# Performance work log

Measured on AMD Instinct MI355X. Metric: run time of the kernel, lower is better.

The kernel has to match this reference:

```python
import jax, jax.numpy as jnp
import numpy as np

N_NODES = 50000
N_EDGES = 800000
D_IN = 256
D_OUT = 128
EPS = 1e-9


def setup_inputs() -> dict:
    key = jax.random.key(0)
    ks = jax.random.split(key, 6)
    feat = jax.random.normal(ks[0], (N_NODES, D_IN), dtype=jnp.float32)
    edge_row = jax.random.randint(ks[1], (N_EDGES,), 0, N_NODES)
    edge_col = jax.random.randint(ks[2], (N_EDGES,), 0, N_NODES)
    # normalized adjacency values (positive, ~1/degree scale)
    edge_val = jax.random.uniform(ks[3], (N_EDGES,), dtype=jnp.float32) / 16.0
    # xavier_uniform for Linear(dim_in, dim_out) weights, stored as [D_IN, D_OUT]
    limit = float(np.sqrt(6.0 / (D_IN + D_OUT)))
    W0 = jax.random.uniform(ks[4], (D_IN, D_OUT), minval=-limit, maxval=limit, dtype=jnp.float32)
    W1 = jax.random.uniform(ks[5], (D_IN, D_OUT), minval=-limit, maxval=limit, dtype=jnp.float32)
    zeros = jnp.zeros((D_OUT,), dtype=jnp.float32)
    ones = jnp.ones((D_OUT,), dtype=jnp.float32)
    return {
        "feat": feat,
        "W0": W0, "b0": zeros, "scale0": ones, "offset0": zeros,
        "W1": W1, "b1": zeros, "scale1": ones, "offset1": zeros,
        "edge_row": edge_row, "edge_col": edge_col, "edge_val": edge_val,
    }


def _spmm(edge_row, edge_col, edge_val, x):
    # out[r] += val * x[c] for each edge (r, c, val)  -- sparse adj @ x
    msgs = edge_val[:, None] * x[edge_col]  # [E, D]
    return jax.ops.segment_sum(msgs, edge_row, num_segments=N_NODES)


def _feat_trans(x, W, b, scale, offset):
    h = jax.nn.relu(x @ W + b)  # [N, D_OUT]
    mean = jnp.mean(h, axis=1, keepdims=True)
    var = jnp.var(h, axis=1, keepdims=True) + EPS  # unbiased=False (population var)
    return (h - mean) * scale * jax.lax.rsqrt(var) + offset


def reference(feat, W0, b0, scale0, offset0, W1, b1, scale1, offset1,
              edge_row, edge_col, edge_val):
    # non-first-layer path: feat_hop = [X, A @ X] (order=1), dropout p=0 is identity
    hop1 = _spmm(edge_row, edge_col, edge_val, feat)
    f0 = _feat_trans(feat, W0, b0, scale0, offset0)
    f1 = _feat_trans(hop1, W1, b1, scale1, offset1)
    return jnp.concatenate([f0, f1], axis=1)  # aggr == 'concat'
```

## Files before the change

### kernel.cpp

```cpp
#include <hip/hip_runtime.h>

#define N_NODES 50000
#define N_EDGES 800000
#define D_IN    256
#define D_OUT   128
#define EPS     1e-9f
#define CAP     64
#define PAD     88

#define SCATTER_BLOCKS 196
#define GEMM_MBLKS     391

typedef __attribute__((ext_vector_type(8))) short bf16x8;
typedef __attribute__((ext_vector_type(4))) float floatx4;

__device__ __forceinline__ ushort f2bf(float x) {
    unsigned u = __float_as_uint(x);
    u += 0x7fffu + ((u >> 16) & 1u);
    return (ushort)(u >> 16);
}

#define CNT_BLOCKS 49
#define WB_BLOCKS  32
__global__ __launch_bounds__(256) void prep_small(
    const float* __restrict__ W0, const float* __restrict__ W1,
    ushort* __restrict__ Wb, int* __restrict__ cnt)
{
    int bid = blockIdx.x;
    int t   = threadIdx.x;
    if (bid < CNT_BLOCKS) {
        int idx4 = bid * 256 + t;
        if (idx4 < 12500)
            *(int4*)&cnt[idx4 * 4] = make_int4(0, 0, 0, 0);
    } else {
        int g  = (bid - CNT_BLOCKS) * 256 + t;
        int n  = g >> 5;
        int kq = g & 31;
        const float* W = (n < 128) ? W0 : W1;
        int nn = n & 127;
        union { ushort us[8]; uint4 v; } tmp;
#pragma unroll
        for (int j = 0; j < 8; ++j)
            tmp.us[j] = f2bf(W[(size_t)(kq * 8 + j) * D_OUT + nn]);
        *(uint4*)&Wb[(size_t)n * D_IN + kq * 8] = tmp.v;
    }
}

__global__ __launch_bounds__(256, 3) void gemm_scatter(
    const float* __restrict__ feat, const ushort* __restrict__ Wb,
    const float* __restrict__ bias, const float* __restrict__ scale,
    const float* __restrict__ offset,
    float* __restrict__ out, ushort* __restrict__ Y1,
    const int* __restrict__ er, const int* __restrict__ ec,
    const float* __restrict__ ev, int* __restrict__ cnt,
    int2* __restrict__ slot2)
{
    __shared__ ushort As[128 * PAD];
    __shared__ ushort Bs[128 * PAD];

    const int t = threadIdx.x;

    if (blockIdx.x < SCATTER_BLOCKS) {
        int ebase = blockIdx.x * 4096;
        int   rr[16], cc[16];
        float vv[16];
#pragma unroll
        for (int u = 0; u < 16; ++u) {
            int e = ebase + u * 256 + t;
            bool ok = (e < N_EDGES);
            rr[u] = ok ? er[e] : -1;
            cc[u] = ok ? ec[e] : 0;
            vv[u] = ok ? ev[e] : 0.f;
        }
#pragma unroll
        for (int u = 0; u < 16; ++u) {
            if (rr[u] >= 0) {
                int pos = atomicAdd(&cnt[rr[u]], 1);
                if (pos < CAP)
                    slot2[(size_t)rr[u] * CAP + pos] =
                        make_int2(cc[u], __float_as_int(vv[u]));
            }
        }
        return;
    }

    const int gbid = blockIdx.x - SCATTER_BLOCKS;
    const int half = gbid / GEMM_MBLKS;
    const int mblk = gbid % GEMM_MBLKS;
    const int wave = t >> 6, lane = t & 63;
    const int quad = lane >> 4, l16 = lane & 15;
    const int m0   = mblk * 128;
    const int n0   = half * 128;

    floatx4 acc[2][8];
#pragma unroll
    for (int mt = 0; mt < 2; ++mt)
#pragma unroll
        for (int nt = 0; nt < 8; ++nt)
            acc[mt][nt] = (floatx4){0.f, 0.f, 0.f, 0.f};

    for (int kt = 0; kt < D_IN; kt += 64) {
#pragma unroll
        for (int i = 0; i < 4; ++i) {
            int g = t + i * 256;
            int row = g >> 3, kq = g & 7;
            int grow = m0 + row;
            union { ushort us[8]; uint4 v; } tmp;
            tmp.v = make_uint4(0u, 0u, 0u, 0u);
            if (grow < N_NODES) {
                const float* p = &feat[(size_t)grow * D_IN + kt + kq * 8];
                float4 v0 = *(const float4*)p;
                float4 v1 = *(const float4*)(p + 4);
                tmp.us[0] = f2bf(v0.x); tmp.us[1] = f2bf(v0.y);
                tmp.us[2] = f2bf(v0.z); tmp.us[3] = f2bf(v0.w);
                tmp.us[4] = f2bf(v1.x); tmp.us[5] = f2bf(v1.y);
                tmp.us[6] = f2bf(v1.z); tmp.us[7] = f2bf(v1.w);
            }
            *(uint4*)&As[row * PAD + kq * 8] = tmp.v;
        }
#pragma unroll
        for (int i = 0; i < 4; ++i) {
            int g = t + i * 256;
            int row = g >> 3, kq = g & 7;
            *(uint4*)&Bs[row * PAD + kq * 8] =
                *(const uint4*)&Wb[(size_t)(n0 + row) * D_IN + kt + kq * 8];
        }
        __syncthreads();

#pragma unroll
        for (int kk = 0; kk < 64; kk += 32) {
            bf16x8 a[2], b[8];
#pragma unroll
            for (int mt = 0; mt < 2; ++mt)
                a[mt] = *(bf16x8*)&As[(wave * 32 + mt * 16 + l16) * PAD + kk + quad * 8];
#pragma unroll
            for (int nt = 0; nt < 8; ++nt)
                b[nt] = *(bf16x8*)&Bs[(nt * 16 + l16) * PAD + kk + quad * 8];
#pragma unroll
            for (int mt = 0; mt < 2; ++mt)
#pragma unroll
                for (int nt = 0; nt < 8; ++nt)
                    acc[mt][nt] = __builtin_amdgcn_mfma_f32_16x16x32_bf16(
                        a[mt], b[nt], acc[mt][nt], 0, 0, 0);
        }
        __syncthreads();
    }

    if (half == 0) {
        float bb[8], sc[8], of[8];
#pragma unroll
        for (int nt = 0; nt < 8; ++nt) {
            bb[nt] = bias[nt * 16 + l16];
            sc[nt] = scale[nt * 16 + l16];
            of[nt] = offset[nt * 16 + l16];
        }
#pragma unroll
        for (int mt = 0; mt < 2; ++mt)
#pragma unroll
            for (int i = 0; i < 4; ++i) {
                float h[8], s = 0.f, q = 0.f;
#pragma unroll
                for (int nt = 0; nt < 8; ++nt) {
                    h[nt] = fmaxf(acc[mt][nt][i] + bb[nt], 0.f);
                    s += h[nt];
                    q += h[nt] * h[nt];
                }
#pragma unroll
                for (int m = 1; m < 16; m <<= 1) {
                    s += __shfl_xor(s, m);
                    q += __shfl_xor(q, m);
                }
                float mean = s * (1.f / 128.f);
                float inv  = rsqrtf(q * (1.f / 128.f) - mean * mean + EPS);
                int row = m0 + wave * 32 + mt * 16 + quad * 4 + i;
                if (row < N_NODES) {
#pragma unroll
                    for (int nt = 0; nt < 8; ++nt)
                        out[(size_t)row * 256 + nt * 16 + l16] =
                            (h[nt] - mean) * sc[nt] * inv + of[nt];
                }
            }
    } else {
#pragma unroll
        for (int mt = 0; mt < 2; ++mt)
#pragma unroll
            for (int i = 0; i < 4; ++i) {
                int row = m0 + wave * 32 + mt * 16 + quad * 4 + i;
                if (row < N_NODES) {
#pragma unroll
                    for (int nt = 0; nt < 8; ++nt)
                        Y1[(size_t)row * D_OUT + nt * 16 + l16] =
                            f2bf(acc[mt][nt][i]);
                }
            }
    }
}

__global__ __launch_bounds__(256) void spmm_gather_ln(
    const int* __restrict__ cnt, const int2* __restrict__ slot2,
    const ushort* __restrict__ Y,
    const float* __restrict__ bias, const float* __restrict__ scale,
    const float* __restrict__ offset, float* __restrict__ out)
{
    int row  = blockIdx.x * 4 + (threadIdx.x >> 6);
    int lane = threadIdx.x & 63;
    if (row >= N_NODES) return;

    int n = cnt[row];
    n = n < CAP ? n : CAP;

    int   c = 0;
    float v = 0.f;
    if (lane < n) {
        int2 p = slot2[(size_t)row * CAP + lane];
        c = p.x;
        v = __int_as_float(p.y);
    }

    float ax = 0.f, ay = 0.f;
    int j = 0;
    for (; j + 8 <= n; j += 8) {
        unsigned yv[8]; float vv[8];
#pragma unroll
        for (int u = 0; u < 8; ++u) {
            int cj = __shfl(c, j + u);
            vv[u]  = __shfl(v, j + u);
            yv[u]  = *(const unsigned*)&Y[(size_t)cj * D_OUT + lane * 2];
        }
#pragma unroll
        for (int u = 0; u < 8; ++u) {
            ax = fmaf(vv[u], __uint_as_float(yv[u] << 16), ax);
            ay = fmaf(vv[u], __uint_as_float(yv[u] & 0xffff0000u), ay);
        }
    }
    for (; j < n; ++j) {
        int   cj = __shfl(c, j);
        float vj = __shfl(v, j);
        unsigned yv = *(const unsigned*)&Y[(size_t)cj * D_OUT + lane * 2];
        ax = fmaf(vj, __uint_as_float(yv << 16), ax);
        ay = fmaf(vj, __uint_as_float(yv & 0xffff0000u), ay);
    }

    int cidx = lane * 2;
    float h0 = fmaxf(ax + bias[cidx + 0], 0.f);
    float h1 = fmaxf(ay + bias[cidx + 1], 0.f);
    float s = h0 + h1, q = h0 * h0 + h1 * h1;
#pragma unroll
    for (int m = 1; m < 64; m <<= 1) {
        s += __shfl_xor(s, m);
        q += __shfl_xor(q, m);
    }
    float mean = s * (1.f / 128.f);
    float var  = q * (1.f / 128.f) - mean * mean + EPS;
    float inv  = rsqrtf(var);
    float2 o;
    o.x = (h0 - mean) * scale[cidx + 0] * inv + offset[cidx + 0];
    o.y = (h1 - mean) * scale[cidx + 1] * inv + offset[cidx + 1];
    *(float2*)&out[(size_t)row * 256 + 128 + cidx] = o;
}

extern "C" void kernel_launch(void* const* d_in, const int* in_sizes, int n_in,
                              void* d_out, int out_size, void* d_ws, size_t ws_size,
                              hipStream_t stream)
{
    const float* feat = (const float*)d_in[0];
    const float* W0   = (const float*)d_in[1];
    const float* b0   = (const float*)d_in[2];
    const float* s0   = (const float*)d_in[3];
    const float* o0   = (const float*)d_in[4];
    const float* W1   = (const float*)d_in[5];
    const float* b1   = (const float*)d_in[6];
    const float* s1   = (const float*)d_in[7];
    const float* o1   = (const float*)d_in[8];
    const int*   er   = (const int*)d_in[9];
    const int*   ec   = (const int*)d_in[10];
    const float* ev   = (const float*)d_in[11];
    float* out = (float*)d_out;

    char*   wsb   = (char*)d_ws;
    ushort* Wb    = (ushort*)(wsb);
    ushort* Y1    = (ushort*)(wsb + 131072);
    int*    cnt   = (int*)   (wsb + 12931072);
    int2*   slot2 = (int2*)  (wsb + 13131072);

    prep_small<<<CNT_BLOCKS + WB_BLOCKS, 256, 0, stream>>>(W0, W1, Wb, cnt);

    gemm_scatter<<<SCATTER_BLOCKS + 2 * GEMM_MBLKS, 256, 0, stream>>>(
        feat, Wb, b0, s0, o0, out, Y1, er, ec, ev, cnt, slot2);

    spmm_gather_ln<<<(N_NODES + 3) / 4, 256, 0, stream>>>(
        cnt, slot2, Y1, b1, s1, o1, out);
}
```

Before: 204.0 us.

## Bucket edges by 128-row groups with shared-memory histogram and local CSR build

Replaces the per-row global atomic slot scatter with a two-level scheme. Each scatter block builds a shared-memory histogram over 128-row buckets, reserves space with one global atomic per bucket, and writes packed (local row, column, value) entries. The gather kernel then loads one bucket into LDS, builds a CSR layout with a prefix scan, and processes its rows. This is meant to cut global atomic contention and the sparse 64-slot-per-row memory footprint, at the cost of extra LDS passes and synchronisation. It also packs the column into 16 bits, which silently assumes node indices below 65536, and a fixed bucket capacity can drop edges.

```diff
diff --git a/kernel.cpp b/kernel.cpp
--- a/kernel.cpp
+++ b/kernel.cpp
@@ -5,11 +5,14 @@
 #define D_IN    256
 #define D_OUT   128
 #define EPS     1e-9f
-#define CAP     64
 #define PAD     88
 
 #define SCATTER_BLOCKS 196
 #define GEMM_MBLKS     391
+
+#define RPB    128
+#define NBUCK  391
+#define BCAP   2560
 
 typedef __attribute__((ext_vector_type(8))) short bf16x8;
 typedef __attribute__((ext_vector_type(4))) float floatx4;
@@ -20,20 +23,17 @@
     return (ushort)(u >> 16);
 }
 
-#define CNT_BLOCKS 49
 #define WB_BLOCKS  32
 __global__ __launch_bounds__(256) void prep_small(
     const float* __restrict__ W0, const float* __restrict__ W1,
-    ushort* __restrict__ Wb, int* __restrict__ cnt)
+    ushort* __restrict__ Wb, int* __restrict__ gcnt)
 {
     int bid = blockIdx.x;
     int t   = threadIdx.x;
-    if (bid < CNT_BLOCKS) {
-        int idx4 = bid * 256 + t;
-        if (idx4 < 12500)
-            *(int4*)&cnt[idx4 * 4] = make_int4(0, 0, 0, 0);
+    if (bid == 0) {
+        for (int i = t; i < NBUCK; i += 256) gcnt[i] = 0;
     } else {
-        int g  = (bid - CNT_BLOCKS) * 256 + t;
+        int g  = (bid - 1) * 256 + t;
         int n  = g >> 5;
         int kq = g & 31;
         const float* W = (n < 128) ? W0 : W1;
@@ -52,8 +52,8 @@
     const float* __restrict__ offset,
     float* __restrict__ out, ushort* __restrict__ Y1,
     const int* __restrict__ er, const int* __restrict__ ec,
-    const float* __restrict__ ev, int* __restrict__ cnt,
-    int2* __restrict__ slot2)
+    const float* __restrict__ ev, int* __restrict__ gcnt,
+    uint2* __restrict__ bedge)
 {
     __shared__ ushort As[128 * PAD];
     __shared__ ushort Bs[128 * PAD];
@@ -61,24 +61,38 @@
     const int t = threadIdx.x;
 
     if (blockIdx.x < SCATTER_BLOCKS) {
+        int* hist = (int*)As;
+        int* base = (int*)Bs;
+        for (int i = t; i < NBUCK; i += 256) hist[i] = 0;
+        __syncthreads();
+
         int ebase = blockIdx.x * 4096;
-        int   rr[16], cc[16];
-        float vv[16];
+        int   bkt[16], rnk[16];
+        uint2 pk[16];
 #pragma unroll
         for (int u = 0; u < 16; ++u) {
             int e = ebase + u * 256 + t;
             bool ok = (e < N_EDGES);
-            rr[u] = ok ? er[e] : -1;
-            cc[u] = ok ? ec[e] : 0;
-            vv[u] = ok ? ev[e] : 0.f;
-        }
+            int   r = ok ? er[e] : 0;
+            int   c = ok ? ec[e] : 0;
+            float v = ok ? ev[e] : 0.f;
+            bkt[u] = ok ? (r >> 7) : -1;
+            pk[u]  = make_uint2(((unsigned)(r & 127) << 16) | (unsigned)c,
+                                __float_as_uint(v));
+            if (ok) rnk[u] = atomicAdd(&hist[r >> 7], 1);
+        }
+        __syncthreads();
+        for (int i = t; i < NBUCK; i += 256) {
+            int h = hist[i];
+            base[i] = h ? atomicAdd(&gcnt[i], h) : 0;
+        }
+        __syncthreads();
 #pragma unroll
         for (int u = 0; u < 16; ++u) {
-            if (rr[u] >= 0) {
-                int pos = atomicAdd(&cnt[rr[u]], 1);
-                if (pos < CAP)
-                    slot2[(size_t)rr[u] * CAP + pos] =
-                        make_int2(cc[u], __float_as_int(vv[u]));
+            if (bkt[u] >= 0) {
+                int pos = base[bkt[u]] + rnk[u];
+                if (pos < BCAP)
+                    bedge[(size_t)bkt[u] * BCAP + pos] = pk[u];
             }
         }
         return;
@@ -196,67 +210,102 @@
     }
 }
 
-__global__ __launch_bounds__(256) void spmm_gather_ln(
-    const int* __restrict__ cnt, const int2* __restrict__ slot2,
+__global__ __launch_bounds__(512) void spmm_gather_ln(
+    const int* __restrict__ gcnt, const uint2* __restrict__ bedge,
     const ushort* __restrict__ Y,
     const float* __restrict__ bias, const float* __restrict__ scale,
     const float* __restrict__ offset, float* __restrict__ out)
 {
-    int row  = blockIdx.x * 4 + (threadIdx.x >> 6);
-    int lane = threadIdx.x & 63;
-    if (row >= N_NODES) return;
-
-    int n = cnt[row];
-    n = n < CAP ? n : CAP;
-
-    int   c = 0;
-    float v = 0.f;
-    if (lane < n) {
-        int2 p = slot2[(size_t)row * CAP + lane];
-        c = p.x;
-        v = __int_as_float(p.y);
-    }
-
-    float ax = 0.f, ay = 0.f;
-    int j = 0;
-    for (; j + 8 <= n; j += 8) {
-        unsigned yv[8]; float vv[8];
-#pragma unroll
-        for (int u = 0; u < 8; ++u) {
-            int cj = __shfl(c, j + u);
-            vv[u]  = __shfl(v, j + u);
-            yv[u]  = *(const unsigned*)&Y[(size_t)cj * D_OUT + lane * 2];
-        }
-#pragma unroll
-        for (int u = 0; u < 8; ++u) {
-            ax = fmaf(vv[u], __uint_as_float(yv[u] << 16), ax);
-            ay = fmaf(vv[u], __uint_as_float(yv[u] & 0xffff0000u), ay);
-        }
-    }
-    for (; j < n; ++j) {
-        int   cj = __shfl(c, j);
-        float vj = __shfl(v, j);
-        unsigned yv = *(const unsigned*)&Y[(size_t)cj * D_OUT + lane * 2];
-        ax = fmaf(vj, __uint_as_float(yv << 16), ax);
-        ay = fmaf(vj, __uint_as_float(yv & 0xffff0000u), ay);
-    }
-
-    int cidx = lane * 2;
-    float h0 = fmaxf(ax + bias[cidx + 0], 0.f);
-    float h1 = fmaxf(ay + bias[cidx + 1], 0.f);
-    float s = h0 + h1, q = h0 * h0 + h1 * h1;
-#pragma unroll
-    for (int m = 1; m < 64; m <<= 1) {
-        s += __shfl_xor(s, m);
-        q += __shfl_xor(q, m);
-    }
-    float mean = s * (1.f / 128.f);
-    float var  = q * (1.f / 128.f) - mean * mean + EPS;
-    float inv  = rsqrtf(var);
-    float2 o;
-    o.x = (h0 - mean) * scale[cidx + 0] * inv + offset[cidx + 0];
-    o.y = (h1 - mean) * scale[cidx + 1] * inv + offset[cidx + 1];
-    *(float2*)&out[(size_t)row * 256 + 128 + cidx] = o;
+    __shared__ int    cnt[RPB];
+    __shared__ int    offx[RPB];
+    __shared__ int    pos[RPB];
+    __shared__ ushort lcol[BCAP];
+    __shared__ float  lval[BCAP];
+
+    const int t      = threadIdx.x;
+    const int bucket = blockIdx.x;
+    const int r0     = bucket * RPB;
+    const int nrows  = min(RPB, N_NODES - r0);
+    int ne = gcnt[bucket];
+    ne = ne < BCAP ? ne : BCAP;
+
+    if (t < RPB) cnt[t] = 0;
+    __syncthreads();
+    for (int i = t; i < ne; i += 512) {
+        uint2 p = bedge[(size_t)bucket * BCAP + i];
+        atomicAdd(&cnt[p.x >> 16], 1);
+    }
+    __syncthreads();
+    if (t < RPB) offx[t] = cnt[t];
+    __syncthreads();
+    for (int s = 1; s < RPB; s <<= 1) {
+        int w = 0;
+        if (t < RPB && t >= s) w = offx[t - s];
+        __syncthreads();
+        if (t < RPB) offx[t] += w;
+        __syncthreads();
+    }
+    if (t < RPB) {
+        offx[t] -= cnt[t];
+        pos[t]   = offx[t];
+    }
+    __syncthreads();
+    for (int i = t; i < ne; i += 512) {
+        uint2 p = bedge[(size_t)bucket * BCAP + i];
+        int r = p.x >> 16;
+        int k = atomicAdd(&pos[r], 1);
+        lcol[k] = (ushort)(p.x & 0xffffu);
+        lval[k] = __uint_as_float(p.y);
+    }
+    __syncthreads();
+
+    const int wave = t >> 6, lane = t & 63;
+    const int cidx = lane * 2;
+    const float b0v = bias[cidx],   b1v = bias[cidx + 1];
+    const float s0v = scale[cidx],  s1v = scale[cidx + 1];
+    const float o0v = offset[cidx], o1v = offset[cidx + 1];
+
+    for (int ri = wave; ri < nrows; ri += 8) {
+        int beg = offx[ri], n = cnt[ri];
+        float ax = 0.f, ay = 0.f;
+        int j = 0;
+        for (; j + 8 <= n; j += 8) {
+            unsigned yv[8]; float vv[8]; int cc[8];
+#pragma unroll
+            for (int u = 0; u < 8; ++u) {
+                cc[u] = lcol[beg + j + u];
+                vv[u] = lval[beg + j + u];
+                yv[u] = *(const unsigned*)&Y[(size_t)cc[u] * D_OUT + cidx];
+            }
+#pragma unroll
+            for (int u = 0; u < 8; ++u) {
+                ax = fmaf(vv[u], __uint_as_float(yv[u] << 16), ax);
+                ay = fmaf(vv[u], __uint_as_float(yv[u] & 0xffff0000u), ay);
+            }
+        }
+        for (; j < n; ++j) {
+            int   c  = lcol[beg + j];
+            float vj = lval[beg + j];
+            unsigned yv = *(const unsigned*)&Y[(size_t)c * D_OUT + cidx];
+            ax = fmaf(vj, __uint_as_float(yv << 16), ax);
+            ay = fmaf(vj, __uint_as_float(yv & 0xffff0000u), ay);
+        }
+        float h0 = fmaxf(ax + b0v, 0.f);
+        float h1 = fmaxf(ay + b1v, 0.f);
+        float s = h0 + h1, q = h0 * h0 + h1 * h1;
+#pragma unroll
+        for (int m = 1; m < 64; m <<= 1) {
+            s += __shfl_xor(s, m);
+            q += __shfl_xor(q, m);
+        }
+        float mean = s * (1.f / 128.f);
+        float inv  = rsqrtf(q * (1.f / 128.f) - mean * mean + EPS);
+        int row = r0 + ri;
+        float2 o;
+        o.x = (h0 - mean) * s0v * inv + o0v;
+        o.y = (h1 - mean) * s1v * inv + o1v;
+        *(float2*)&out[(size_t)row * 256 + 128 + cidx] = o;
+    }
 }
 
 extern "C" void kernel_launch(void* const* d_in, const int* in_sizes, int n_in,
@@ -280,14 +329,14 @@
     char*   wsb   = (char*)d_ws;
     ushort* Wb    = (ushort*)(wsb);
     ushort* Y1    = (ushort*)(wsb + 131072);
-    int*    cnt   = (int*)   (wsb + 12931072);
-    int2*   slot2 = (int2*)  (wsb + 13131072);
-
-    prep_small<<<CNT_BLOCKS + WB_BLOCKS, 256, 0, stream>>>(W0, W1, Wb, cnt);
+    int*    gcnt  = (int*)   (wsb + 12931072);
+    uint2*  bedge = (uint2*) (wsb + 12932672);
+
+    prep_small<<<1 + WB_BLOCKS, 256, 0, stream>>>(W0, W1, Wb, gcnt);
 
     gemm_scatter<<<SCATTER_BLOCKS + 2 * GEMM_MBLKS, 256, 0, stream>>>(
-        feat, Wb, b0, s0, o0, out, Y1, er, ec, ev, cnt, slot2);
-
-    spmm_gather_ln<<<(N_NODES + 3) / 4, 256, 0, stream>>>(
-        cnt, slot2, Y1, b1, s1, o1, out);
-}
+        feat, Wb, b0, s0, o0, out, Y1, er, ec, ev, gcnt, bedge);
+
+    spmm_gather_ln<<<NBUCK, 512, 0, stream>>>(
+        gcnt, bedge, Y1, b1, s1, o1, out);
+}
```

Result: faster. 192.7 us (-5.6%).
